# Kernel optimization log

Hardware: AMD Instinct MI355X
Metric: run time of the kernel (lower is better)

The kernel has to match this reference:

```python
import jax, jax.numpy as jnp
import numpy as np

B, T, D = 2, 2048, 1024
H, HS = 16, 64
EPS = 1e-5

def _ln(x, g, b):
    m = jnp.mean(x, axis=-1, keepdims=True)
    v = jnp.mean((x - m) ** 2, axis=-1, keepdims=True)
    return (x - m) * jax.lax.rsqrt(v + EPS) * g + b

def setup_inputs() -> dict:
    key = jax.random.key(0)
    ks = jax.random.split(key, 8)
    s_in = 1.0 / np.sqrt(D)
    s_ff = 1.0 / np.sqrt(4 * D)
    return {
        "embds": jax.random.normal(ks[0], (B, T, D), jnp.float32),
        "Wq": jax.random.normal(ks[1], (H, D, HS), jnp.float32) * s_in,
        "Wk": jax.random.normal(ks[2], (H, D, HS), jnp.float32) * s_in,
        "Wv": jax.random.normal(ks[3], (H, D, HS), jnp.float32) * s_in,
        "ln1_g": jnp.ones((D,), jnp.float32),
        "ln1_b": jnp.zeros((D,), jnp.float32),
        "ln2_g": jnp.ones((D,), jnp.float32),
        "ln2_b": jnp.zeros((D,), jnp.float32),
        "W1": jax.random.normal(ks[4], (D, 4 * D), jnp.float32) * s_in,
        "b1": jnp.zeros((4 * D,), jnp.float32),
        "W2": jax.random.normal(ks[5], (4 * D, D), jnp.float32) * s_ff,
        "b2": jnp.zeros((D,), jnp.float32),
    }

def reference(embds, Wq, Wk, Wv, ln1_g, ln1_b, ln2_g, ln2_b, W1, b1, W2, b2):
    _, t, d = embds.shape
    x = _ln(embds, ln1_g, ln1_b)
    q = jnp.einsum("btd,hde->bhte", x, Wq)
    k = jnp.einsum("btd,hde->bhte", x, Wk)
    v = jnp.einsum("btd,hde->bhte", x, Wv)
    # NOTE: repo scales by num_embds**-0.5 (C of input), not head_size**-0.5
    scores = jnp.einsum("bhte,bhse->bhts", q, k) * (d ** -0.5)
    causal = jnp.tril(jnp.ones((t, t), bool))
    scores = jnp.where(causal, scores, -jnp.inf)
    w = jax.nn.softmax(scores, axis=-1)
    o = jnp.einsum("bhts,bhse->bhte", w, v)  # [B,H,T,HS]
    attn = o.transpose(0, 2, 1, 3).reshape(embds.shape[0], t, -1)  # concat heads
    embds = embds + attn
    y = _ln(embds, ln2_g, ln2_b)
    ff = jax.nn.relu(y @ W1 + b1) @ W2 + b2
    return embds + ff
```

## Files before the change

### kernel.cpp

```cpp
#include <hip/hip_runtime.h>

using s16x8 = __attribute__((ext_vector_type(8))) short;
using f32x4 = __attribute__((ext_vector_type(4))) float;
typedef unsigned int   u32;
typedef unsigned short u16;

__device__ __forceinline__ u16 f2bf(float f) {
  u32 u = __float_as_uint(f);
  u += 0x7fffu + ((u >> 16) & 1u);
  return (u16)(u >> 16);
}
__device__ __forceinline__ float bf2f(u16 s) {
  return __uint_as_float(((u32)s) << 16);
}

typedef __attribute__((address_space(1))) const unsigned int g_u32;
typedef __attribute__((address_space(3))) unsigned int l_u32;
__device__ __forceinline__ void gload16(const void* g, void* l) {
  __builtin_amdgcn_global_load_lds((g_u32*)g, (l_u32*)l, 16, 0, 0);
}

#define WAITB(N) asm volatile("s_waitcnt vmcnt(" #N ")\ns_barrier" ::: "memory")

__device__ __forceinline__ size_t kfrag_addr(int bh, int t, int e) {
  const int pair = (((t >> 4) & 3) << 1) + (e >> 5);
  const int slot = ((e >> 3) & 3) * 16 + (t & 15);
  return ((((size_t)bh * 32 + (t >> 6)) * 8 + pair) * 64 + slot) * 8 + (e & 7);
}
__device__ __forceinline__ size_t vfrag_addr(int bh, int t, int e) {
  const int pair = (((e >> 4) & 3) << 1) + ((t >> 5) & 1);
  const int slot = ((t >> 3) & 3) * 16 + (e & 15);
  return ((((size_t)bh * 32 + (t >> 6)) * 8 + pair) * 64 + slot) * 8 + (t & 7);
}

__global__ __launch_bounds__(256) void transpose_pack(
    const float* __restrict__ src, u16* __restrict__ dst, int R, int C)
{
  __shared__ u16 tile[64][66];
  const int tid = threadIdx.x;
  const int c0 = blockIdx.x * 64, r0 = blockIdx.y * 64;
  const size_t zoff = (size_t)blockIdx.z * R * C;
  src += zoff; dst += zoff;
  const int rr = tid >> 6, cc = tid & 63;
  #pragma unroll
  for (int i = 0; i < 16; ++i)
    tile[i * 4 + rr][cc] = f2bf(src[(size_t)(r0 + i * 4 + rr) * C + c0 + cc]);
  __syncthreads();
  #pragma unroll
  for (int i = 0; i < 16; ++i)
    dst[(size_t)(c0 + i * 4 + rr) * R + r0 + cc] = tile[cc][i * 4 + rr];
}

__global__ __launch_bounds__(256) void transpose_qkv(
    const float* __restrict__ Wq, const float* __restrict__ Wk,
    const float* __restrict__ Wv, u16* __restrict__ dst)
{
  __shared__ u16 tile[64][66];
  const int tid = threadIdx.x;
  const int sel = blockIdx.z >> 4, head = blockIdx.z & 15;
  const int r0 = blockIdx.y * 64;
  const float* src = ((sel == 0) ? Wq : (sel == 1) ? Wk : Wv) + (size_t)head * 65536;
  u16* d = dst + ((size_t)sel << 20) + (size_t)head * 65536;
  const int rr = tid >> 6, cc = tid & 63;
  #pragma unroll
  for (int i = 0; i < 16; ++i)
    tile[i * 4 + rr][cc] = f2bf(src[(size_t)(r0 + i * 4 + rr) * 64 + cc]);
  __syncthreads();
  #pragma unroll
  for (int i = 0; i < 16; ++i)
    d[(size_t)(i * 4 + rr) * 1024 + r0 + cc] = tile[cc][i * 4 + rr];
}

__global__ __launch_bounds__(256) void ln_kernel(
    const float* __restrict__ x, const float* __restrict__ g,
    const float* __restrict__ be, u16* __restrict__ out)
{
  const int row = blockIdx.x, tid = threadIdx.x;
  const int lane = tid & 63, wave = tid >> 6;
  const float4 v = ((const float4*)(x + (size_t)row * 1024))[tid];
  float s  = v.x + v.y + v.z + v.w;
  float sq = v.x * v.x + v.y * v.y + v.z * v.z + v.w * v.w;
  #pragma unroll
  for (int m = 1; m < 64; m <<= 1) { s += __shfl_xor(s, m); sq += __shfl_xor(sq, m); }
  __shared__ float rs[4], rq[4];
  if (lane == 0) { rs[wave] = s; rq[wave] = sq; }
  __syncthreads();
  s  = rs[0] + rs[1] + rs[2] + rs[3];
  sq = rq[0] + rq[1] + rq[2] + rq[3];
  const float mean = s * (1.0f / 1024.0f);
  const float var  = sq * (1.0f / 1024.0f) - mean * mean;
  const float rstd = rsqrtf(var + 1e-5f);
  const int c = tid * 4;
  const float4 gv = ((const float4*)g)[tid];
  const float4 bv = ((const float4*)be)[tid];
  ushort4 o;
  o.x = f2bf((v.x - mean) * rstd * gv.x + bv.x);
  o.y = f2bf((v.y - mean) * rstd * gv.y + bv.y);
  o.z = f2bf((v.z - mean) * rstd * gv.z + bv.z);
  o.w = f2bf((v.w - mean) * rstd * gv.w + bv.w);
  *(ushort4*)&out[(size_t)row * 1024 + c] = o;
}

template<int MODE, int MR>
__global__ __launch_bounds__(256) void gemm128(
    const u16* __restrict__ A, const u16* __restrict__ BT, int K,
    u16* __restrict__ o0q, u16* __restrict__ o0k, u16* __restrict__ o0v,
    u16* __restrict__ o1, const float* __restrict__ bias,
    float* __restrict__ o2, const float* __restrict__ resid)
{
  constexpr int BM = 64 * MR;
  __shared__ alignas(16) u16 As[3][BM * 32];
  __shared__ alignas(16) u16 Bs[3][128 * 32];
  const int tid = threadIdx.x, lane = tid & 63, wave = tid >> 6;
  const int wr = wave >> 1, wc = wave & 1;
  const int gx = gridDim.x;
  const int nwg = gx * gridDim.y;
  int lid = blockIdx.y * gx + blockIdx.x;
  lid = (lid & 7) * (nwg >> 3) + (lid >> 3);
  const int row0 = (lid / gx) * BM, col0 = (lid % gx) * 128;
  const int fr = lane & 15, g = lane >> 4;
  const int swz = (g ^ ((fr >> 1) & 3)) * 8;

  const int sr = wave * 16 + (lane >> 2);
  const int sc = ((lane & 3) ^ ((lane >> 3) & 3)) * 8;
  const u16* Ap0 = A  + (size_t)(row0 + sr) * K + sc;
  const u16* Ap1 = A  + (size_t)(row0 + 64 + sr) * K + sc;
  const u16* Bp0 = BT + (size_t)(col0 + sr) * K + sc;
  const u16* Bp1 = BT + (size_t)(col0 + 64 + sr) * K + sc;

  f32x4 acc[2 * MR][4] = {};

  auto stage = [&](int sel, int k0) {
    gload16(Ap0 + k0, &As[sel][wave * 512]);
    if constexpr (MR == 2) gload16(Ap1 + k0, &As[sel][(4 + wave) * 512]);
    gload16(Bp0 + k0, &Bs[sel][wave * 512]);
    gload16(Bp1 + k0, &Bs[sel][(4 + wave) * 512]);
  };
  auto compute = [&](int sel) {
    s16x8 af[2 * MR], bfr[4];
    #pragma unroll
    for (int m = 0; m < 2 * MR; ++m)
      af[m] = *(const s16x8*)&As[sel][(wr * (32 * MR) + m * 16 + fr) * 32 + swz];
    #pragma unroll
    for (int n = 0; n < 4; ++n)
      bfr[n] = *(const s16x8*)&Bs[sel][(wc * 64 + n * 16 + fr) * 32 + swz];
    #pragma unroll
    for (int m = 0; m < 2 * MR; ++m)
      #pragma unroll
      for (int n = 0; n < 4; ++n)
        acc[m][n] = __builtin_amdgcn_mfma_f32_16x16x32_bf16(af[m], bfr[n], acc[m][n], 0, 0, 0);
  };

  const int nsteps = K / 32;
  stage(0, 0);
  stage(1, 32);
  int cur = 0;
  for (int t = 0; t < nsteps - 1; ++t) {
    if constexpr (MR == 2) WAITB(4); else WAITB(3);
    const int nxt = (cur == 2) ? 0 : cur + 1;
    const int nn  = (nxt == 2) ? 0 : nxt + 1;
    if (t + 2 < nsteps) stage(nn, (t + 2) * 32);
    compute(cur);
    cur = nxt;
  }
  WAITB(0);
  compute(cur);

  const float QSCALE = 0.03125f * 1.4426950408889634f;
  #pragma unroll
  for (int m = 0; m < 2 * MR; ++m) {
    const int rbase = row0 + wr * (32 * MR) + m * 16 + g * 4;
    #pragma unroll
    for (int n = 0; n < 4; ++n) {
      const int col = col0 + wc * 64 + n * 16 + fr;
      if constexpr (MODE == 0) {
        const int w = col >> 10, h = (col >> 6) & 15, e = col & 63;
        const int b = rbase >> 11, t0 = rbase & 2047;
        const int bh = b * 16 + h;
        if (w == 0) {
          #pragma unroll
          for (int j = 0; j < 4; ++j)
            o0q[((size_t)bh * 2048 + (t0 + j)) * 64 + e] = f2bf(acc[m][n][j] * QSCALE);
        } else if (w == 1) {
          #pragma unroll
          for (int j = 0; j < 4; ++j)
            o0k[kfrag_addr(bh, t0 + j, e)] = f2bf(acc[m][n][j]);
        } else {
          ushort4 pk;
          pk.x = f2bf(acc[m][n][0]); pk.y = f2bf(acc[m][n][1]);
          pk.z = f2bf(acc[m][n][2]); pk.w = f2bf(acc[m][n][3]);
          *(ushort4*)&o0v[vfrag_addr(bh, t0, e)] = pk;
        }
      } else if constexpr (MODE == 1) {
        const float bb = bias[col];
        #pragma unroll
        for (int j = 0; j < 4; ++j) {
          float v = fmaxf(acc[m][n][j] + bb, 0.0f);
          o1[(size_t)(rbase + j) * 4096 + col] = f2bf(v);
        }
      } else {
        const float bb = bias[col];
        #pragma unroll
        for (int j = 0; j < 4; ++j) {
          const size_t ix = (size_t)(rbase + j) * 1024 + col;
          o2[ix] = acc[m][n][j] + bb + resid[ix];
        }
      }
    }
  }
}

__global__ __launch_bounds__(256) void attn_mfma(
    const u16* __restrict__ q, const u16* __restrict__ kfragG,
    const u16* __restrict__ vfragG, const float* __restrict__ embds,
    float* __restrict__ e2)
{
  __shared__ alignas(16) u16 kbuf[3][4096];
  __shared__ alignas(16) u16 vbuf[3][4096];
  __shared__ alignas(16) u16 p_sm[4][16][72];
  const int tid = threadIdx.x, lane = tid & 63, wave = tid >> 6;
  const int bh = blockIdx.x & 31;
  const int qb = 31 - (blockIdx.x >> 5);
  const int q0 = qb * 64 + wave * 16;
  const int b = bh >> 4, h = bh & 15;
  const int fr = lane & 15, g = lane >> 4;

  const u16* qp = q + ((size_t)bh * 2048 + q0 + fr) * 64 + g * 8;
  const s16x8 qf0 = *(const s16x8*)(qp);
  const s16x8 qf1 = *(const s16x8*)(qp + 32);

  f32x4 o_acc[4] = {};
  float lacc[4] = {};

  const size_t fragbase = (size_t)bh * 131072;
  const int p0 = wave * 2, p1 = wave * 2 + 1;
  const int nch = qb + 1;

  auto stage_kv = [&](int sel, int c) {
    const size_t cb = fragbase + (size_t)c * 4096;
    gload16(kfragG + cb + p0 * 512 + lane * 8, &kbuf[sel][p0 * 512]);
    gload16(kfragG + cb + p1 * 512 + lane * 8, &kbuf[sel][p1 * 512]);
    gload16(vfragG + cb + p0 * 512 + lane * 8, &vbuf[sel][p0 * 512]);
    gload16(vfragG + cb + p1 * 512 + lane * 8, &vbuf[sel][p1 * 512]);
  };
  auto compute = [&](int sel, int s0) {
    f32x4 sacc[4] = {};
    #pragma unroll
    for (int n = 0; n < 4; ++n) {
      const s16x8 kf0 = *(const s16x8*)&kbuf[sel][(n * 2 + 0) * 512 + lane * 8];
      const s16x8 kf1 = *(const s16x8*)&kbuf[sel][(n * 2 + 1) * 512 + lane * 8];
      sacc[n] = __builtin_amdgcn_mfma_f32_16x16x32_bf16(qf0, kf0, sacc[n], 0, 0, 0);
      sacc[n] = __builtin_amdgcn_mfma_f32_16x16x32_bf16(qf1, kf1, sacc[n], 0, 0, 0);
    }
    if (s0 + 63 > q0) {
      #pragma unroll
      for (int n = 0; n < 4; ++n) {
        const int s = s0 + n * 16 + fr;
        #pragma unroll
        for (int j = 0; j < 4; ++j)
          if (s > q0 + g * 4 + j) sacc[n][j] = -1e30f;
      }
    }
    float p[4][4];
    #pragma unroll
    for (int n = 0; n < 4; ++n)
      #pragma unroll
      for (int j = 0; j < 4; ++j) {
        p[n][j] = __builtin_amdgcn_exp2f(sacc[n][j]);
        lacc[j] += p[n][j];
      }
    #pragma unroll
    for (int n = 0; n < 4; ++n)
      #pragma unroll
      for (int j = 0; j < 4; ++j)
        p_sm[wave][g * 4 + j][n * 16 + fr] = f2bf(p[n][j]);
    const s16x8 pf0 = *(const s16x8*)&p_sm[wave][fr][g * 8];
    const s16x8 pf1 = *(const s16x8*)&p_sm[wave][fr][32 + g * 8];
    #pragma unroll
    for (int n = 0; n < 4; ++n) {
      const s16x8 vf0 = *(const s16x8*)&vbuf[sel][(n * 2 + 0) * 512 + lane * 8];
      const s16x8 vf1 = *(const s16x8*)&vbuf[sel][(n * 2 + 1) * 512 + lane * 8];
      o_acc[n] = __builtin_amdgcn_mfma_f32_16x16x32_bf16(pf0, vf0, o_acc[n], 0, 0, 0);
      o_acc[n] = __builtin_amdgcn_mfma_f32_16x16x32_bf16(pf1, vf1, o_acc[n], 0, 0, 0);
    }
  };

  stage_kv(0, 0);
  if (nch > 1) stage_kv(1, 1);
  int cur = 0;
  for (int t = 0; t < nch - 1; ++t) {
    WAITB(4);
    const int nxt = (cur == 2) ? 0 : cur + 1;
    const int nn  = (nxt == 2) ? 0 : nxt + 1;
    if (t + 2 < nch) stage_kv(nn, t + 2);
    compute(cur, t * 64);
    cur = nxt;
  }
  WAITB(0);
  compute(cur, (nch - 1) * 64);

  #pragma unroll
  for (int j = 0; j < 4; ++j) {
    #pragma unroll
    for (int mm = 1; mm < 16; mm <<= 1) lacc[j] += __shfl_xor(lacc[j], mm);
  }

  #pragma unroll
  for (int n = 0; n < 4; ++n) {
    #pragma unroll
    for (int j = 0; j < 4; ++j) {
      const int t = q0 + g * 4 + j;
      const size_t oi = ((size_t)b * 2048 + t) * 1024 + (size_t)h * 64 + n * 16 + fr;
      e2[oi] = embds[oi] + o_acc[n][j] / lacc[j];
    }
  }
}

extern "C" void kernel_launch(void* const* d_in, const int* in_sizes, int n_in,
                              void* d_out, int out_size, void* d_ws, size_t ws_size,
                              hipStream_t stream) {
  const float* embds = (const float*)d_in[0];
  const float* Wq    = (const float*)d_in[1];
  const float* Wk    = (const float*)d_in[2];
  const float* Wv    = (const float*)d_in[3];
  const float* ln1g  = (const float*)d_in[4];
  const float* ln1b  = (const float*)d_in[5];
  const float* ln2g  = (const float*)d_in[6];
  const float* ln2b  = (const float*)d_in[7];
  const float* W1    = (const float*)d_in[8];
  const float* b1    = (const float*)d_in[9];
  const float* W2    = (const float*)d_in[10];
  const float* b2    = (const float*)d_in[11];
  float* out = (float*)d_out;

  char* ws = (char*)d_ws;
  u16*   xln   = (u16*)(ws);
  u16*   wqkvT = (u16*)(ws + (8ull  << 20));
  u16*   qbuf  = (u16*)(ws + (14ull << 20));
  u16*   kfrag = (u16*)(ws + (22ull << 20));
  u16*   vfrag = (u16*)(ws + (30ull << 20));
  float* e2    = (float*)(ws + (38ull << 20));
  u16*   ybuf  = (u16*)(ws + (54ull << 20));
  u16*   w1T   = (u16*)(ws + (62ull << 20));
  u16*   w2T   = (u16*)(ws + (70ull << 20));
  u16*   hid   = (u16*)(ws + (78ull << 20));

  transpose_qkv<<<dim3(1, 16, 48), 256, 0, stream>>>(Wq, Wk, Wv, wqkvT);
  transpose_pack<<<dim3(64, 16, 1), 256, 0, stream>>>(W1, w1T, 1024, 4096);
  transpose_pack<<<dim3(16, 64, 1), 256, 0, stream>>>(W2, w2T, 4096, 1024);
  ln_kernel<<<4096, 256, 0, stream>>>(embds, ln1g, ln1b, xln);
  gemm128<0, 2><<<dim3(24, 32), 256, 0, stream>>>(xln, wqkvT, 1024,
      qbuf, kfrag, vfrag, nullptr, nullptr, nullptr, nullptr);
  attn_mfma<<<1024, 256, 0, stream>>>(qbuf, kfrag, vfrag, embds, e2);
  ln_kernel<<<4096, 256, 0, stream>>>(e2, ln2g, ln2b, ybuf);
  gemm128<1, 2><<<dim3(32, 32), 256, 0, stream>>>(ybuf, w1T, 1024,
      nullptr, nullptr, nullptr, hid, b1, nullptr, nullptr);
  gemm128<2, 1><<<dim3(8, 64), 256, 0, stream>>>(hid, w2T, 4096,
      nullptr, nullptr, nullptr, nullptr, b2, out, e2);
}
```

Before: 225.2 us.

## Use 256x256-tile 8-wave GEMM for FFN with split-K FF2 and reduce

Replaces the two FFN GEMMs with a new 512-thread kernel that computes 256x256 output tiles from double-buffered, XOR-swizzled LDS. It interleaves LDS fragment reads, async global-to-LDS staging and MFMA quarters, separated by barriers and raised wave priority around the MFMAs. FF2 is split 4-way over K, writing bf16 partials into reused workspace, and a new reduce kernel adds the partials, bias and residual. The aim is more data reuse per tile and full CU coverage for FF2. In exchange the partial sums are rounded to bf16 and there is an extra pass over memory.

```diff
diff --git a/kernel.cpp b/kernel.cpp
--- a/kernel.cpp
+++ b/kernel.cpp
@@ -21,6 +21,7 @@
 }
 
 #define WAITB(N) asm volatile("s_waitcnt vmcnt(" #N ")\ns_barrier" ::: "memory")
+#define BAR()    asm volatile("s_barrier" ::: "memory")
 
 __device__ __forceinline__ size_t kfrag_addr(int bh, int t, int e) {
   const int pair = (((t >> 4) & 3) << 1) + (e >> 5);
@@ -101,6 +102,158 @@
   *(ushort4*)&out[(size_t)row * 1024 + c] = o;
 }
 
+#define MFMA_Q(MQ, NH)                                                        \
+  do {                                                                        \
+    __builtin_amdgcn_s_setprio(1);                                            \
+    _Pragma("unroll") for (int m_ = 0; m_ < 4; ++m_)                          \
+      _Pragma("unroll") for (int n_ = 0; n_ < 2; ++n_)                        \
+        _Pragma("unroll") for (int ks_ = 0; ks_ < 2; ++ks_)                   \
+          acc[MQ * 4 + m_][NH * 2 + n_] =                                     \
+            __builtin_amdgcn_mfma_f32_16x16x32_bf16(                          \
+              aF[m_][ks_], (NH ? b1F : b0F)[n_][ks_],                         \
+              acc[MQ * 4 + m_][NH * 2 + n_], 0, 0, 0);                        \
+    __builtin_amdgcn_s_setprio(0);                                            \
+  } while (0)
+
+template<int MODE>
+__global__ __launch_bounds__(512, 2) void gemm256(
+    const u16* __restrict__ A, int lda, const u16* __restrict__ BT, int ldb,
+    int K, u16* __restrict__ o1, const float* __restrict__ bias,
+    u16* __restrict__ pout)
+{
+  __shared__ alignas(16) u16 lds[2][2][256 * 64];
+  const int tid = threadIdx.x, lane = tid & 63, w = tid >> 6;
+  const int wm = w >> 2, wn = w & 3;
+  const int fr = lane & 15, g = lane >> 4;
+  const int gx = gridDim.x, nwg = gx * gridDim.y;
+  int lid = blockIdx.y * gx + blockIdx.x;
+  lid = (lid & 7) * (nwg >> 3) + (lid >> 3);
+  const int col0 = (lid % gx) * 256, row0 = (lid / gx) * 256;
+  const int koff = (MODE == 3) ? blockIdx.z * 1024 : 0;
+  if constexpr (MODE == 3) pout += (size_t)blockIdx.z * (4096 * 1024);
+
+  const int srow = w * 16 + (lane >> 3);
+  const int scol8 = (lane & 7) ^ ((lane >> 3) & 7);
+  const u16* Ab = A  + (size_t)(row0 + srow) * lda + koff + scol8 * 8;
+  const u16* Bb = BT + (size_t)(col0 + srow) * ldb + koff + scol8 * 8;
+  const int sdst = (w * 16) * 64 + lane * 8;
+
+  const int x7 = fr & 7;
+  const int rA = wm * 128 + fr;
+  const int rB = wn * 64 + fr;
+
+  f32x4 acc[8][4] = {};
+  s16x8 aF[4][2], b0F[2][2], b1F[2][2];
+  const int nkt = K >> 6;
+
+  auto stA = [&](int buf, int half, int kt) {
+    #pragma unroll
+    for (int g2 = 0; g2 < 2; ++g2)
+      gload16(Ab + (size_t)(half * 128 + g2 * 8) * lda + kt * 64,
+              &lds[buf][0][(half * 128 + g2 * 8) * 64 + sdst]);
+  };
+  auto stB = [&](int buf, int half, int kt) {
+    #pragma unroll
+    for (int g2 = 0; g2 < 2; ++g2)
+      gload16(Bb + (size_t)(half * 128 + g2 * 8) * ldb + kt * 64,
+              &lds[buf][1][(half * 128 + g2 * 8) * 64 + sdst]);
+  };
+  auto rdA = [&](int buf, int mq) {
+    #pragma unroll
+    for (int m = 0; m < 4; ++m)
+      #pragma unroll
+      for (int ks = 0; ks < 2; ++ks)
+        aF[m][ks] = *(const s16x8*)
+          &lds[buf][0][(rA + mq * 64 + m * 16) * 64 + ((ks * 4 + g) ^ x7) * 8];
+  };
+  auto rdB0 = [&](int buf) {
+    #pragma unroll
+    for (int n = 0; n < 2; ++n)
+      #pragma unroll
+      for (int ks = 0; ks < 2; ++ks)
+        b0F[n][ks] = *(const s16x8*)
+          &lds[buf][1][(rB + n * 16) * 64 + ((ks * 4 + g) ^ x7) * 8];
+  };
+  auto rdB1 = [&](int buf) {
+    #pragma unroll
+    for (int n = 0; n < 2; ++n)
+      #pragma unroll
+      for (int ks = 0; ks < 2; ++ks)
+        b1F[n][ks] = *(const s16x8*)
+          &lds[buf][1][(rB + (n + 2) * 16) * 64 + ((ks * 4 + g) ^ x7) * 8];
+  };
+
+  stA(0, 0, 0); stA(0, 1, 0); stB(0, 0, 0); stB(0, 1, 0);
+  stA(1, 0, 1); stA(1, 1, 1); stB(1, 0, 1); stB(1, 1, 1);
+  WAITB(8);
+
+  const int niter = nkt >> 1;
+  for (int i = 0; i < niter; ++i) {
+    #pragma unroll
+    for (int half = 0; half < 2; ++half) {
+      const int buf = half;
+      const int skt = 2 * i + 2 + half;
+      const bool st = (skt < nkt);
+      rdA(buf, 0); rdB0(buf);
+      BAR();
+      MFMA_Q(0, 0);
+      BAR();
+      rdB1(buf);
+      if (st) stB(buf, 0, skt);
+      BAR();
+      MFMA_Q(0, 1);
+      BAR();
+      rdA(buf, 1);
+      if (st) stA(buf, 0, skt);
+      BAR();
+      MFMA_Q(1, 0);
+      BAR();
+      if (st) { stA(buf, 1, skt); stB(buf, 1, skt); }
+      BAR();
+      MFMA_Q(1, 1);
+      WAITB(6);
+    }
+  }
+
+  #pragma unroll
+  for (int m8 = 0; m8 < 8; ++m8) {
+    const int rbase = row0 + wm * 128 + m8 * 16 + g * 4;
+    #pragma unroll
+    for (int n4 = 0; n4 < 4; ++n4) {
+      const int col = col0 + wn * 64 + n4 * 16 + fr;
+      if constexpr (MODE == 1) {
+        const float bb = bias[col];
+        #pragma unroll
+        for (int j = 0; j < 4; ++j)
+          o1[(size_t)(rbase + j) * 4096 + col] =
+            f2bf(fmaxf(acc[m8][n4][j] + bb, 0.0f));
+      } else {
+        #pragma unroll
+        for (int j = 0; j < 4; ++j)
+          pout[(size_t)(rbase + j) * 1024 + col] = f2bf(acc[m8][n4][j]);
+      }
+    }
+  }
+}
+
+__global__ __launch_bounds__(256) void ff2_reduce(
+    const u16* __restrict__ pbuf, const float* __restrict__ e2,
+    const float* __restrict__ b2, float* __restrict__ out)
+{
+  const int i4 = blockIdx.x * 256 + threadIdx.x;
+  const int row = i4 >> 8, c4 = i4 & 255;
+  float4 a = ((const float4*)e2)[i4];
+  const float4 bb = ((const float4*)b2)[c4];
+  a.x += bb.x; a.y += bb.y; a.z += bb.z; a.w += bb.w;
+  #pragma unroll
+  for (int z = 0; z < 4; ++z) {
+    const ushort4 p = *(const ushort4*)
+      &pbuf[(size_t)z * (4096 * 1024) + (size_t)row * 1024 + c4 * 4];
+    a.x += bf2f(p.x); a.y += bf2f(p.y); a.z += bf2f(p.z); a.w += bf2f(p.w);
+  }
+  ((float4*)out)[i4] = a;
+}
+
 template<int MODE, int MR>
 __global__ __launch_bounds__(256) void gemm128(
     const u16* __restrict__ A, const u16* __restrict__ BT, int K,
@@ -174,14 +327,14 @@
     for (int n = 0; n < 4; ++n) {
       const int col = col0 + wc * 64 + n * 16 + fr;
       if constexpr (MODE == 0) {
-        const int w = col >> 10, h = (col >> 6) & 15, e = col & 63;
+        const int ww = col >> 10, h = (col >> 6) & 15, e = col & 63;
         const int b = rbase >> 11, t0 = rbase & 2047;
         const int bh = b * 16 + h;
-        if (w == 0) {
+        if (ww == 0) {
           #pragma unroll
           for (int j = 0; j < 4; ++j)
             o0q[((size_t)bh * 2048 + (t0 + j)) * 64 + e] = f2bf(acc[m][n][j] * QSCALE);
-        } else if (w == 1) {
+        } else if (ww == 1) {
           #pragma unroll
           for (int j = 0; j < 4; ++j)
             o0k[kfrag_addr(bh, t0 + j, e)] = f2bf(acc[m][n][j]);
@@ -304,7 +457,6 @@
     #pragma unroll
     for (int mm = 1; mm < 16; mm <<= 1) lacc[j] += __shfl_xor(lacc[j], mm);
   }
-
   #pragma unroll
   for (int n = 0; n < 4; ++n) {
     #pragma unroll
@@ -335,6 +487,7 @@
 
   char* ws = (char*)d_ws;
   u16*   xln   = (u16*)(ws);
+  u16*   pbuf  = (u16*)(ws);
   u16*   wqkvT = (u16*)(ws + (8ull  << 20));
   u16*   qbuf  = (u16*)(ws + (14ull << 20));
   u16*   kfrag = (u16*)(ws + (22ull << 20));
@@ -353,8 +506,9 @@
       qbuf, kfrag, vfrag, nullptr, nullptr, nullptr, nullptr);
   attn_mfma<<<1024, 256, 0, stream>>>(qbuf, kfrag, vfrag, embds, e2);
   ln_kernel<<<4096, 256, 0, stream>>>(e2, ln2g, ln2b, ybuf);
-  gemm128<1, 2><<<dim3(32, 32), 256, 0, stream>>>(ybuf, w1T, 1024,
-      nullptr, nullptr, nullptr, hid, b1, nullptr, nullptr);
-  gemm128<2, 1><<<dim3(8, 64), 256, 0, stream>>>(hid, w2T, 4096,
-      nullptr, nullptr, nullptr, nullptr, b2, out, e2);
-}
+  gemm256<1><<<dim3(16, 16), 512, 0, stream>>>(ybuf, 1024, w1T, 1024, 1024,
+      hid, b1, nullptr);
+  gemm256<3><<<dim3(4, 16, 4), 512, 0, stream>>>(hid, 4096, w2T, 4096, 1024,
+      nullptr, nullptr, pbuf);
+  ff2_reduce<<<4096, 256, 0, stream>>>(pbuf, e2, b2, out);
+}
```

New measurement: 190.6 us. 1.18x faster.
